# Optimization experiments

Hardware: AMD Instinct MI355X
Metric: run time of the kernel (lower is better)

Reference implementation:

```python
import jax, jax.numpy as jnp
import numpy as np

DMODEL = 1024
H = 16
DK = DMODEL // H  # 64
B, L = 4, 4096


def setup_inputs() -> dict:
    key = jax.random.key(0)
    ks = jax.random.split(key, 9)
    Q = jax.random.normal(ks[0], (B, L, DMODEL), dtype=jnp.float32)
    K = jax.random.normal(ks[1], (B, L, DMODEL), dtype=jnp.float32)
    V = jax.random.normal(ks[2], (B, L, DMODEL), dtype=jnp.float32)
    s = 1.0 / np.sqrt(DMODEL)
    Wq = jax.random.normal(ks[3], (DMODEL, DK), dtype=jnp.float32) * s
    Wk = jax.random.normal(ks[4], (DMODEL, DK), dtype=jnp.float32) * s
    Wv = jax.random.normal(ks[5], (DMODEL, DK), dtype=jnp.float32) * s
    bq = jnp.zeros((DK,), jnp.float32)
    bk = jnp.zeros((DK,), jnp.float32)
    bv = jnp.zeros((DK,), jnp.float32)
    # causal self-attention mask: True where attention is DISALLOWED (masked_fill semantics)
    causal = ~jnp.tril(jnp.ones((L, L), dtype=bool))  # [L, L]
    mask_self_attention = jnp.broadcast_to(causal, (B, L, L))
    return {"Q": Q, "K": K, "V": V, "Wq": Wq, "bq": bq, "Wk": Wk, "bk": bk,
            "Wv": Wv, "bv": bv, "mask_self_attention": mask_self_attention}


def reference(Q, K, V, Wq, bq, Wk, bk, Wv, bv, mask_self_attention):
    # per-head linear projections: [B, L, dmodel] -> [B, L, dk]
    q = jnp.einsum('bld,dk->blk', Q, Wq) + bq
    k = jnp.einsum('bld,dk->blk', K, Wk) + bk
    v = jnp.einsum('bld,dk->blk', V, Wv) + bv
    # scores: [B, L, L]
    scores = jnp.einsum('blk,bmk->blm', q, k) / jnp.sqrt(jnp.float32(DK))
    scores = jnp.where(mask_self_attention, -jnp.inf, scores)
    attn = jax.nn.softmax(scores, axis=-1)
    # dropout_rate = 0.0 -> identity
    return jnp.einsum('blm,bmk->blk', attn, v)
```

## Files before the change

### kernel.cpp

```cpp
#include <hip/hip_runtime.h>
#include <hip/hip_bf16.h>
#include <math.h>

#define DM 1024
#define DKx 64
#define NB 4
#define LL 4096
#define MTOT (NB * LL)

typedef __attribute__((ext_vector_type(8))) __bf16 bf16x8;
typedef __attribute__((ext_vector_type(4))) __bf16 bf16x4;
typedef __attribute__((ext_vector_type(4))) float f32x4;

#define SCALE_LOG2E 0.18033688011112042f

__device__ __forceinline__ f32x4 mfma16(bf16x8 a, bf16x8 b, f32x4 c) {
  return __builtin_amdgcn_mfma_f32_16x16x32_bf16(a, b, c, 0, 0, 0);
}

extern "C" __global__ __launch_bounds__(256) void proj_kernel(
    const float* __restrict__ Xq, const float* __restrict__ Xk, const float* __restrict__ Xv,
    const float* __restrict__ Wq, const float* __restrict__ Wk, const float* __restrict__ Wv,
    const float* __restrict__ bq, const float* __restrict__ bk, const float* __restrict__ bv,
    __bf16* __restrict__ qo, __bf16* __restrict__ ko, __bf16* __restrict__ vTo)
{
  const int which = blockIdx.y;
  const float* X    = (which == 0) ? Xq : (which == 1) ? Xk : Xv;
  const float* W    = (which == 0) ? Wq : (which == 1) ? Wk : Wv;
  const float* bias = (which == 0) ? bq : (which == 1) ? bk : bv;

  __shared__ __bf16 sWt[64 * 72];

  const int tid  = threadIdx.x;
  const int wave = tid >> 6;
  const int lane = tid & 63;
  const int quad = lane >> 4;
  const int c    = lane & 15;
  const int rowbase = blockIdx.x * 64;
  const int arow = rowbase + wave * 16 + c;

  f32x4 acc[4];
#pragma unroll
  for (int t = 0; t < 4; ++t) acc[t] = (f32x4){0.f, 0.f, 0.f, 0.f};

  const int sn   = tid & 63;
  const int slot = tid >> 6;

  for (int kk = 0; kk < DM; kk += 64) {
    __syncthreads();
#pragma unroll
    for (int p = 0; p < 4; ++p) {
      const int r0 = slot * 4 + p * 16;
      bf16x4 pk;
#pragma unroll
      for (int i = 0; i < 4; ++i)
        pk[i] = (__bf16)W[(kk + r0 + i) * DKx + sn];
      *reinterpret_cast<bf16x4*>(&sWt[sn * 72 + r0]) = pk;
    }
    __syncthreads();

    bf16x8 af[2];
#pragma unroll
    for (int s = 0; s < 2; ++s) {
      const float* src = X + (size_t)arow * DM + kk + s * 32 + quad * 8;
      float4 u0 = *reinterpret_cast<const float4*>(src);
      float4 u1 = *reinterpret_cast<const float4*>(src + 4);
      bf16x8 a;
      a[0] = (__bf16)u0.x; a[1] = (__bf16)u0.y; a[2] = (__bf16)u0.z; a[3] = (__bf16)u0.w;
      a[4] = (__bf16)u1.x; a[5] = (__bf16)u1.y; a[6] = (__bf16)u1.z; a[7] = (__bf16)u1.w;
      af[s] = a;
    }
#pragma unroll
    for (int t = 0; t < 4; ++t) {
      bf16x8 b0 = *reinterpret_cast<const bf16x8*>(&sWt[(t * 16 + c) * 72 + quad * 8]);
      bf16x8 b1 = *reinterpret_cast<const bf16x8*>(&sWt[(t * 16 + c) * 72 + 32 + quad * 8]);
      acc[t] = mfma16(af[0], b0, acc[t]);
      acc[t] = mfma16(af[1], b1, acc[t]);
    }
  }

#pragma unroll
  for (int t = 0; t < 4; ++t) {
    const int col = t * 16 + c;
    const float bb = bias[col];
#pragma unroll
    for (int r = 0; r < 4; ++r) {
      float v = acc[t][r] + bb;
      if (which == 0) v *= SCALE_LOG2E;
      const int row = rowbase + wave * 16 + quad * 4 + r;
      const __bf16 h = (__bf16)v;
      if (which == 0)      qo[(size_t)row * DKx + col] = h;
      else if (which == 1) ko[(size_t)row * DKx + col] = h;
      else                 vTo[((size_t)(row >> 12) * DKx + col) * LL + (row & (LL - 1))] = h;
    }
  }
}

extern "C" __global__ __launch_bounds__(256) void attn_kernel(
    const __bf16* __restrict__ qws, const __bf16* __restrict__ kws,
    const __bf16* __restrict__ vTws, float* __restrict__ out)
{
  const int tile = blockIdx.x;
  const int b    = blockIdx.y;
  const int tid  = threadIdx.x;
  const int wave = tid >> 6;
  const int lane = tid & 63;
  const int quad = lane >> 4;
  const int c    = lane & 15;
  const int qbase = tile * 64;

  __shared__ __bf16 sK[64 * 72];
  __shared__ __bf16 sVt[64 * 72];
  __shared__ __bf16 sP[64 * 72];

  bf16x8 qf[2];
  {
    const __bf16* qp = qws + (size_t)(b * LL + qbase + wave * 16 + c) * DKx + quad * 8;
    qf[0] = *reinterpret_cast<const bf16x8*>(qp);
    qf[1] = *reinterpret_cast<const bf16x8*>(qp + 32);
  }

  f32x4 o[4];
#pragma unroll
  for (int t = 0; t < 4; ++t) o[t] = (f32x4){0.f, 0.f, 0.f, 0.f};
  float m_[4], l_[4];
#pragma unroll
  for (int r = 0; r < 4; ++r) { m_[r] = -1e30f; l_[r] = 0.f; }

  const int rr0 = tid >> 3;
  const int seg = tid & 7;

  for (int j = 0; j <= tile; ++j) {
    const int n0 = j * 64;
    __syncthreads();
    {
      const __bf16* kp = kws + (size_t)(b * LL + n0 + rr0) * DKx + seg * 8;
      *reinterpret_cast<bf16x8*>(&sK[rr0 * 72 + seg * 8]) =
          *reinterpret_cast<const bf16x8*>(kp);
      *reinterpret_cast<bf16x8*>(&sK[(rr0 + 32) * 72 + seg * 8]) =
          *reinterpret_cast<const bf16x8*>(kp + 32 * DKx);
      const __bf16* vp = vTws + (size_t)(b * DKx + rr0) * LL + n0 + seg * 8;
      *reinterpret_cast<bf16x8*>(&sVt[rr0 * 72 + seg * 8]) =
          *reinterpret_cast<const bf16x8*>(vp);
      *reinterpret_cast<bf16x8*>(&sVt[(rr0 + 32) * 72 + seg * 8]) =
          *reinterpret_cast<const bf16x8*>(vp + (size_t)32 * LL);
    }
    __syncthreads();

    f32x4 s[4];
#pragma unroll
    for (int t = 0; t < 4; ++t) {
      bf16x8 b0 = *reinterpret_cast<const bf16x8*>(&sK[(t * 16 + c) * 72 + quad * 8]);
      bf16x8 b1 = *reinterpret_cast<const bf16x8*>(&sK[(t * 16 + c) * 72 + 32 + quad * 8]);
      f32x4 z = (f32x4){0.f, 0.f, 0.f, 0.f};
      z = mfma16(qf[0], b0, z);
      s[t] = mfma16(qf[1], b1, z);
    }

    if (j == tile) {
#pragma unroll
      for (int t = 0; t < 4; ++t)
#pragma unroll
        for (int r = 0; r < 4; ++r)
          if (t * 16 + c > wave * 16 + quad * 4 + r) s[t][r] = -1e30f;
    }

    float mc[4], alpha[4], psum[4];
#pragma unroll
    for (int r = 0; r < 4; ++r)
      mc[r] = fmaxf(fmaxf(s[0][r], s[1][r]), fmaxf(s[2][r], s[3][r]));
#pragma unroll
    for (int r = 0; r < 4; ++r) {
      mc[r] = fmaxf(mc[r], __shfl_xor(mc[r], 1));
      mc[r] = fmaxf(mc[r], __shfl_xor(mc[r], 2));
      mc[r] = fmaxf(mc[r], __shfl_xor(mc[r], 4));
      mc[r] = fmaxf(mc[r], __shfl_xor(mc[r], 8));
    }
#pragma unroll
    for (int r = 0; r < 4; ++r) {
      const float mn = fmaxf(m_[r], mc[r]);
      alpha[r] = __builtin_amdgcn_exp2f(m_[r] - mn);
      m_[r] = mn;
      psum[r] = 0.f;
    }
#pragma unroll
    for (int t = 0; t < 4; ++t)
#pragma unroll
      for (int r = 0; r < 4; ++r) {
        const float p = __builtin_amdgcn_exp2f(s[t][r] - m_[r]);
        s[t][r] = p;
        psum[r] += p;
      }
#pragma unroll
    for (int r = 0; r < 4; ++r) {
      psum[r] += __shfl_xor(psum[r], 1);
      psum[r] += __shfl_xor(psum[r], 2);
      psum[r] += __shfl_xor(psum[r], 4);
      psum[r] += __shfl_xor(psum[r], 8);
      l_[r] = l_[r] * alpha[r] + psum[r];
    }

#pragma unroll
    for (int t = 0; t < 4; ++t)
#pragma unroll
      for (int r = 0; r < 4; ++r) {
        sP[(wave * 16 + quad * 4 + r) * 72 + t * 16 + c] = (__bf16)s[t][r];
        o[t][r] *= alpha[r];
      }

    bf16x8 pf0 = *reinterpret_cast<const bf16x8*>(&sP[(wave * 16 + c) * 72 + quad * 8]);
    bf16x8 pf1 = *reinterpret_cast<const bf16x8*>(&sP[(wave * 16 + c) * 72 + 32 + quad * 8]);
#pragma unroll
    for (int t = 0; t < 4; ++t) {
      bf16x8 v0 = *reinterpret_cast<const bf16x8*>(&sVt[(t * 16 + c) * 72 + quad * 8]);
      bf16x8 v1 = *reinterpret_cast<const bf16x8*>(&sVt[(t * 16 + c) * 72 + 32 + quad * 8]);
      o[t] = mfma16(pf0, v0, o[t]);
      o[t] = mfma16(pf1, v1, o[t]);
    }
  }

#pragma unroll
  for (int r = 0; r < 4; ++r) {
    const float inv = 1.f / l_[r];
    const int row = qbase + wave * 16 + quad * 4 + r;
#pragma unroll
    for (int t = 0; t < 4; ++t)
      out[(size_t)(b * LL + row) * DKx + t * 16 + c] = o[t][r] * inv;
  }
}

extern "C" void kernel_launch(void* const* d_in, const int* in_sizes, int n_in,
                              void* d_out, int out_size, void* d_ws, size_t ws_size,
                              hipStream_t stream)
{
  const float* Q  = (const float*)d_in[0];
  const float* K  = (const float*)d_in[1];
  const float* V  = (const float*)d_in[2];
  const float* Wq = (const float*)d_in[3];
  const float* bq = (const float*)d_in[4];
  const float* Wk = (const float*)d_in[5];
  const float* bk = (const float*)d_in[6];
  const float* Wv = (const float*)d_in[7];
  const float* bv = (const float*)d_in[8];
  float* out = (float*)d_out;

  __bf16* qws = (__bf16*)d_ws;
  __bf16* kws = qws + (size_t)MTOT * DKx;
  __bf16* vT  = kws + (size_t)MTOT * DKx;

  proj_kernel<<<dim3(MTOT / 64, 3), 256, 0, stream>>>(
      Q, K, V, Wq, Wk, Wv, bq, bk, bv, qws, kws, vT);
  attn_kernel<<<dim3(LL / 64, NB), 256, 0, stream>>>(qws, kws, vT, out);
}
```

Baseline: 545.0 us.

## Split causal attention KV range into chunks with a separate combine kernel

The attention kernel splits each query tile's causal KV loop into chunks of 8 key blocks spread over a third grid dimension. Each chunk writes its unnormalized partial output plus running max and sum to workspace. A new combine kernel merges the partials with log-sum-exp weighting. This is meant to fix the load imbalance and low parallelism of the causal loop, where late tiles ran up to 64 iterations on only 256 blocks. The cost is extra partial-result memory traffic, an extra kernel launch, and many early-exiting blocks.

```diff
diff --git a/kernel.cpp b/kernel.cpp
--- a/kernel.cpp
+++ b/kernel.cpp
@@ -7,6 +7,9 @@
 #define NB 4
 #define LL 4096
 #define MTOT (NB * LL)
+
+#define CHUNK 8
+#define NCH 8
 
 typedef __attribute__((ext_vector_type(8))) __bf16 bf16x8;
 typedef __attribute__((ext_vector_type(4))) __bf16 bf16x4;
@@ -96,12 +99,18 @@
   }
 }
 
-extern "C" __global__ __launch_bounds__(256) void attn_kernel(
+extern "C" __global__ __launch_bounds__(256, 4) void attn_kernel(
     const __bf16* __restrict__ qws, const __bf16* __restrict__ kws,
-    const __bf16* __restrict__ vTws, float* __restrict__ out)
+    const __bf16* __restrict__ vTws, float* __restrict__ Opart,
+    float* __restrict__ mpart, float* __restrict__ lpart)
 {
   const int tile = blockIdx.x;
   const int b    = blockIdx.y;
+  const int s_ch = blockIdx.z;
+  if (s_ch * CHUNK > tile) return;
+  const int jbeg = s_ch * CHUNK;
+  const int jend = min(tile + 1, jbeg + CHUNK);
+
   const int tid  = threadIdx.x;
   const int wave = tid >> 6;
   const int lane = tid & 63;
@@ -130,7 +139,7 @@
   const int rr0 = tid >> 3;
   const int seg = tid & 7;
 
-  for (int j = 0; j <= tile; ++j) {
+  for (int j = jbeg; j < jend; ++j) {
     const int n0 = j * 64;
     __syncthreads();
     {
@@ -219,13 +228,64 @@
     }
   }
 
+  float* Op = Opart + (((size_t)(b * 64 + tile) * NCH + s_ch) * 64 * 64);
 #pragma unroll
   for (int r = 0; r < 4; ++r) {
-    const float inv = 1.f / l_[r];
-    const int row = qbase + wave * 16 + quad * 4 + r;
+    const int rl = wave * 16 + quad * 4 + r;
 #pragma unroll
     for (int t = 0; t < 4; ++t)
-      out[(size_t)(b * LL + row) * DKx + t * 16 + c] = o[t][r] * inv;
+      Op[rl * 64 + t * 16 + c] = o[t][r];
+    if (c == 0) {
+      const size_t mi = ((size_t)(b * 64 + tile) * NCH + s_ch) * 64 + rl;
+      mpart[mi] = m_[r];
+      lpart[mi] = l_[r];
+    }
+  }
+}
+
+extern "C" __global__ __launch_bounds__(256) void combine_kernel(
+    const float* __restrict__ Opart, const float* __restrict__ mpart,
+    const float* __restrict__ lpart, float* __restrict__ out)
+{
+  const int tile = blockIdx.x;
+  const int b    = blockIdx.y;
+  const int nch  = tile / CHUNK + 1;
+  const int tid  = threadIdx.x;
+  const int row  = tid >> 2;
+  const int cg   = tid & 3;
+  const size_t base = (size_t)(b * 64 + tile) * NCH;
+
+  float m = -1e30f;
+  for (int s = 0; s < nch; ++s)
+    m = fmaxf(m, mpart[(base + s) * 64 + row]);
+  float w[NCH];
+  float denom = 0.f;
+  for (int s = 0; s < nch; ++s) {
+    w[s] = __builtin_amdgcn_exp2f(mpart[(base + s) * 64 + row] - m);
+    denom += w[s] * lpart[(base + s) * 64 + row];
+  }
+  const float inv = 1.f / denom;
+
+  f32x4 acc[4];
+#pragma unroll
+  for (int i = 0; i < 4; ++i) acc[i] = (f32x4){0.f, 0.f, 0.f, 0.f};
+  for (int s = 0; s < nch; ++s) {
+    const f32x4* op = reinterpret_cast<const f32x4*>(
+        Opart + (base + s) * 64 * 64 + row * 64 + cg * 16);
+#pragma unroll
+    for (int i = 0; i < 4; ++i) {
+      f32x4 v = op[i];
+#pragma unroll
+      for (int e = 0; e < 4; ++e) acc[i][e] += w[s] * v[e];
+    }
+  }
+  float* dst = out + (size_t)(b * LL + tile * 64 + row) * DKx + cg * 16;
+#pragma unroll
+  for (int i = 0; i < 4; ++i) {
+    f32x4 v;
+#pragma unroll
+    for (int e = 0; e < 4; ++e) v[e] = acc[i][e] * inv;
+    reinterpret_cast<f32x4*>(dst)[i] = v;
   }
 }
 
@@ -247,8 +307,13 @@
   __bf16* qws = (__bf16*)d_ws;
   __bf16* kws = qws + (size_t)MTOT * DKx;
   __bf16* vT  = kws + (size_t)MTOT * DKx;
+  float* Opart = (float*)(vT + (size_t)MTOT * DKx);
+  float* mpart = Opart + (size_t)NB * 64 * NCH * 64 * 64;
+  float* lpart = mpart + (size_t)NB * 64 * NCH * 64;
 
   proj_kernel<<<dim3(MTOT / 64, 3), 256, 0, stream>>>(
       Q, K, V, Wq, Wk, Wv, bq, bk, bv, qws, kws, vT);
-  attn_kernel<<<dim3(LL / 64, NB), 256, 0, stream>>>(qws, kws, vT, out);
-}
+  attn_kernel<<<dim3(LL / 64, NB, NCH), 256, 0, stream>>>(
+      qws, kws, vT, Opart, mpart, lpart);
+  combine_kernel<<<dim3(LL / 64, NB), 256, 0, stream>>>(Opart, mpart, lpart, out);
+}
```

New measurement: 489.7 us. -10.2%, faster.
